# Performance work log

Hardware: AMD Instinct MI355X
Metric: run time of the kernel (lower is better)

Reference implementation:

```python
import jax, jax.numpy as jnp
import numpy as np

IMG = 1024
P0, P1 = 32, 16          # patch_size = [32, 16], P0 = 2*P1 required by stride-2 conv
C = 1                    # num_channels (must be 1 for unflatten(encoded, 1) to be valid)
N0 = (IMG // P0) ** 2    # 1024 patches at coarse scale
N1 = (IMG // P1) ** 2    # 4096 patches at fine scale
D0 = C * P0 * P0         # 1024 projection dim (coarse)
D1 = C * P1 * P1         # 256 projection dim (fine)
B = 8
BN_EPS = 1e-3            # keras BatchNormalization default
LRELU_ALPHA = 0.3        # keras LeakyReLU default


def setup_inputs() -> dict:
    key = jax.random.key(0)
    ks = jax.random.split(key, 9)
    return {
        "X": jax.random.normal(ks[0], (B, IMG, IMG, C), jnp.float32),
        "W_emb": jax.random.normal(ks[1], (N0, D0), jnp.float32) * 0.02,
        "conv_w": jax.random.normal(ks[2], (3, 3, N0, N1), jnp.float32) * 0.02,
        "conv_b": jnp.zeros((N1,), jnp.float32),
        "bn_gamma": jax.random.uniform(ks[3], (N1,), jnp.float32) + 0.5,
        "bn_beta": jax.random.normal(ks[4], (N1,), jnp.float32) * 0.1,
        "bn_mean": jax.random.normal(ks[5], (N1,), jnp.float32) * 0.1,
        "bn_var": jax.random.uniform(ks[6], (N1,), jnp.float32) + 0.5,
        "W_dense": jax.random.normal(ks[7], (D0, D0), jnp.float32) * 0.02,
        "b_dense": jnp.zeros((D0,), jnp.float32),
    }


def _patches(x, p):
    # [B,H,W,C] -> [B, (H/p)*(W/p), p, p, C]; row-major patch order, matching tf split/stack path.
    b, h, w, c = x.shape
    x = x.reshape(b, h // p, p, w // p, p, c).transpose(0, 1, 3, 2, 4, 5)
    return x.reshape(b, (h // p) * (w // p), p, p, c)


def _unpatch(x):
    # [B, n, p, p, C] -> [B, e*p, e*p, C] with e = sqrt(n); exact inverse of _patches.
    b, n, p, _, c = x.shape
    e = int(np.sqrt(n))
    x = x.reshape(b, e, e, p, p, c).transpose(0, 1, 3, 2, 4, 5)
    return x.reshape(b, e * p, e * p, c)


def reference(X, W_emb, conv_w, conv_b, bn_gamma, bn_beta, bn_mean, bn_var, W_dense, b_dense):
    b = X.shape[0]
    # fine-scale patches, flattened
    flat = _patches(X, P1).reshape(b, N1, D1)

    # positional embedding 1: positions = arange(N0) -> full embedding table
    pos1 = W_emb  # [N0, D0]

    # positional embedding 2: unflatten -> conv branch (inference: dropout = identity, BN uses moving stats)
    pe = pos1.reshape(1, N0, P0, P0, C).transpose(0, 4, 2, 3, 1).reshape(C, P0, P0, N0)  # [C,P0,P0,N0]
    y = jax.lax.conv_general_dilated(
        pe, conv_w, window_strides=(2, 2), padding='SAME',
        dimension_numbers=('NHWC', 'HWIO', 'NHWC')) + conv_b            # [C, P1, P1, N1]
    y = (y - bn_mean) * (bn_gamma / jnp.sqrt(bn_var + BN_EPS)) + bn_beta
    y = jnp.where(y > 0, y, LRELU_ALPHA * y)
    pos2 = y.reshape(1, C, P1, P1, N1).transpose(0, 4, 2, 3, 1).reshape(1, N1, D1)

    enc = flat + pos2                                                    # [B, N1, D1]
    # unflatten(.,1) -> unpatch -> repatch at coarse scale (pure reshape/transpose)
    img = _unpatch(enc.reshape(b, N1, P1, P1, 1))                        # [B, IMG, IMG, 1]
    enc = _patches(img, P0).reshape(b, N0, D0) + pos1                    # [B, N0, D0]
    return enc @ W_dense + b_dense
```

## Files before the change

### kernel.cpp

```cpp
#include <hip/hip_runtime.h>

typedef __attribute__((ext_vector_type(8))) short short8;
typedef __attribute__((ext_vector_type(4))) short short4v;
typedef __attribute__((ext_vector_type(4))) float float4v;

typedef const void __attribute__((address_space(1)))* gptr_t;
typedef void __attribute__((address_space(3)))* lptr_t;

__device__ __forceinline__ void gload_lds16(const void* g, void* l) {
    __builtin_amdgcn_global_load_lds((gptr_t)g, (lptr_t)l, 16, 0, 0);
}

__device__ __forceinline__ unsigned short f2bf(float f) {
    union { float f; unsigned int u; } v; v.f = f;
    unsigned int r = v.u + 0x7fffu + ((v.u >> 16) & 1u);
    return (unsigned short)(r >> 16);
}

__device__ __forceinline__ short8 frag_ld(const unsigned char* base, int row, int k2) {
    return *(const short8*)(base + row * 128 + (k2 ^ ((row & 7) << 4)));
}

__device__ __forceinline__ int swzB(int n) {
    return ((n ^ (n >> 3)) & 7) << 4;
}

__device__ __forceinline__ short8 frag_ldB(const unsigned char* base, int n, int k2) {
    return *(const short8*)(base + n * 128 + (k2 ^ swzB(n)));
}

__device__ __forceinline__ float4v mfma_bf16(short8 a, short8 b, float4v c) {
    return __builtin_amdgcn_mfma_f32_16x16x32_bf16(a, b, c, 0, 0, 0);
}

__global__ __launch_bounds__(256) void k_transpose_bf16(
        const float* __restrict__ in, unsigned short* __restrict__ out,
        float* __restrict__ zb) {
    __shared__ float tile[32][33];
    int tx = threadIdx.x, ty = threadIdx.y;
    if (blockIdx.x == 0 && blockIdx.y == 0 && ty == 0) zb[tx] = 0.0f;
    int x = blockIdx.x * 32 + tx;
    int ybase = blockIdx.y * 32;
#pragma unroll
    for (int j = 0; j < 4; j++)
        tile[ty + j * 8][tx] = in[(size_t)(ybase + ty + j * 8) * 1024 + x];
    __syncthreads();
    int ox = ybase + tx;
    int oybase = blockIdx.x * 32;
#pragma unroll
    for (int j = 0; j < 4; j++)
        out[(size_t)(oybase + ty + j * 8) * 1024 + ox] = f2bf(tile[tx][ty + j * 8]);
}

__global__ __launch_bounds__(256, 2) void k_conv_gemm(
        const float* __restrict__ convw,
        const unsigned short* __restrict__ peT,
        const unsigned short* __restrict__ zerobuf,
        float* __restrict__ y_part)
{
    __shared__ __align__(16) unsigned char ldsA[2][16384];
    __shared__ __align__(16) unsigned char ldsB[2][16384];

    const int t = threadIdx.x;
    const int L = blockIdx.x;
    const int ell = (L & 7) * 72 + (L >> 3);
    const int mt = ell & 1;
    const int nt = (ell >> 1) & 31;
    const int s  = ell >> 6;
    const int kh = s / 3, kw = s - kh * 3;
    const int ncol0 = nt * 128;

    const int l = t & 63, w = t >> 6;
    const int wm = w >> 1, wn = w & 1;
    const int l15 = l & 15;
    const int lk2 = (l >> 4) * 16;

    float4v acc[4][4] = {};

    const unsigned short* asrc[4];
    int aok[4];
#pragma unroll
    for (int i = 0; i < 4; i++) {
        int idx = i * 256 + t;
        int r = idx >> 3, c8 = idx & 7;
        int m = mt * 128 + r;
        int oh = m >> 4, ow = m & 15;
        int ih = 2 * oh + kh, iw = 2 * ow + kw;
        bool ok = (ih < 32) && (iw < 32);
        asrc[i] = ok ? (peT + (size_t)(ih * 32 + iw) * 1024 + ((c8 ^ (r & 7)) * 8))
                     : zerobuf;
        aok[i] = ok ? ~0 : 0;
    }

    const int a = t & 15, b = t >> 4;
    const float* bbase = convw + ((size_t)s * 1024 + 4 * a) * 4096 + ncol0 + 4 * b;

    float4v rb[2][2][4];

#pragma unroll
    for (int i = 0; i < 4; i++)
        gload_lds16(asrc[i], &ldsA[0][(i * 256 + t) * 16]);
#pragma unroll
    for (int c = 0; c < 2; c++)
#pragma unroll
        for (int j = 0; j < 4; j++)
            rb[0][c][j] = *(const float4v*)(bbase + (size_t)j * 4096 + c * 64);
    __builtin_amdgcn_sched_barrier(0);
#pragma unroll
    for (int i = 0; i < 4; i++)
        gload_lds16(asrc[i] + (64 & aok[i]), &ldsA[1][(i * 256 + t) * 16]);
#pragma unroll
    for (int c = 0; c < 2; c++)
#pragma unroll
        for (int j = 0; j < 4; j++)
            rb[1][c][j] = *(const float4v*)(bbase + (size_t)(64 + j) * 4096 + c * 64);
    asm volatile("s_waitcnt vmcnt(12)" ::: "memory");
    __builtin_amdgcn_sched_barrier(0);
#pragma unroll
    for (int c = 0; c < 2; c++)
#pragma unroll
        for (int i = 0; i < 4; i++) {
            int n = 4 * b + c * 64 + i;
            short4v v;
            v.x = (short)f2bf(rb[0][c][0][i]);
            v.y = (short)f2bf(rb[0][c][1][i]);
            v.z = (short)f2bf(rb[0][c][2][i]);
            v.w = (short)f2bf(rb[0][c][3][i]);
            *(short4v*)(&ldsB[0][n * 128 + ((a * 8) ^ swzB(n))]) = v;
        }
    asm volatile("s_waitcnt lgkmcnt(0)" ::: "memory");
    __builtin_amdgcn_s_barrier();

#pragma unroll
    for (int tt = 0; tt < 16; ++tt) {
        const int cur = tt & 1;

        short8 af[4][2], bfr[4][2];
#pragma unroll
        for (int mf = 0; mf < 4; mf++)
#pragma unroll
            for (int ks = 0; ks < 2; ks++)
                af[mf][ks] = frag_ld(ldsA[cur], wm * 64 + mf * 16 + l15, ks * 64 + lk2);
#pragma unroll
        for (int nf = 0; nf < 4; nf++)
#pragma unroll
            for (int ks = 0; ks < 2; ks++)
                bfr[nf][ks] = frag_ldB(ldsB[cur], wn * 64 + nf * 16 + l15, ks * 64 + lk2);
        asm volatile("s_waitcnt lgkmcnt(0)" ::: "memory");
        __builtin_amdgcn_sched_barrier(0);
        __builtin_amdgcn_s_barrier();
        __builtin_amdgcn_sched_barrier(0);

        if (tt < 14) {
            const int k0n = (tt + 2) * 64;
#pragma unroll
            for (int i = 0; i < 4; i++)
                gload_lds16(asrc[i] + (k0n & aok[i]), &ldsA[cur][(i * 256 + t) * 16]);
#pragma unroll
            for (int c = 0; c < 2; c++)
#pragma unroll
                for (int j = 0; j < 4; j++)
                    rb[cur][c][j] = *(const float4v*)(bbase + (size_t)(k0n + j) * 4096 + c * 64);
        }

        __builtin_amdgcn_s_setprio(1);
#pragma unroll
        for (int mf = 0; mf < 4; mf++)
#pragma unroll
            for (int nf = 0; nf < 4; nf++)
#pragma unroll
                for (int ks = 0; ks < 2; ks++)
                    acc[mf][nf] = mfma_bf16(af[mf][ks], bfr[nf][ks], acc[mf][nf]);
        __builtin_amdgcn_s_setprio(0);

        if (tt < 15) {
            if (tt < 14) asm volatile("s_waitcnt vmcnt(12)" ::: "memory");
            else         asm volatile("s_waitcnt vmcnt(0)" ::: "memory");
            __builtin_amdgcn_sched_barrier(0);
#pragma unroll
            for (int c = 0; c < 2; c++)
#pragma unroll
                for (int i = 0; i < 4; i++) {
                    int n = 4 * b + c * 64 + i;
                    short4v v;
                    v.x = (short)f2bf(rb[cur ^ 1][c][0][i]);
                    v.y = (short)f2bf(rb[cur ^ 1][c][1][i]);
                    v.z = (short)f2bf(rb[cur ^ 1][c][2][i]);
                    v.w = (short)f2bf(rb[cur ^ 1][c][3][i]);
                    *(short4v*)(&ldsB[cur ^ 1][n * 128 + ((a * 8) ^ swzB(n))]) = v;
                }
            asm volatile("s_waitcnt lgkmcnt(0)" ::: "memory");
            __builtin_amdgcn_sched_barrier(0);
            __builtin_amdgcn_s_barrier();
        }
    }

    float* yp = y_part + (size_t)s * 1048576;
#pragma unroll
    for (int mf = 0; mf < 4; mf++) {
        int row = mt * 128 + wm * 64 + mf * 16 + (l >> 4) * 4;
#pragma unroll
        for (int nf = 0; nf < 4; nf++) {
            int col = ncol0 + wn * 64 + nf * 16 + l15;
#pragma unroll
            for (int rr = 0; rr < 4; rr++)
                yp[(size_t)(row + rr) * 4096 + col] = acc[mf][nf][rr];
        }
    }
}

__global__ __launch_bounds__(256) void k_bn_pos2(
        const float* __restrict__ y_part, const float* __restrict__ cb,
        const float* __restrict__ gamma, const float* __restrict__ beta,
        const float* __restrict__ mean, const float* __restrict__ var,
        float* __restrict__ pos2img) {
    int idx = blockIdx.x * 256 + threadIdx.x;
    int m = idx >> 12, oc = idx & 4095;
    float v = cb[oc];
#pragma unroll
    for (int s = 0; s < 9; s++)
        v += y_part[(size_t)s * 1048576 + idx];
    v = (v - mean[oc]) * (gamma[oc] * rsqrtf(var[oc] + 1e-3f)) + beta[oc];
    v = v > 0.0f ? v : 0.3f * v;
    int y = ((oc >> 6) << 4) + (m >> 4);
    int x = ((oc & 63) << 4) + (m & 15);
    pos2img[y * 1024 + x] = v;
}

__global__ __launch_bounds__(256) void k_build_A(
        const float* __restrict__ X, const float* __restrict__ pos2img,
        const float* __restrict__ W_emb, unsigned short* __restrict__ Aenc) {
    int row = blockIdx.x;
    int n0 = row & 1023;
    int b  = row >> 10;
    int d0 = threadIdx.x * 4;
    int y = ((n0 >> 5) << 5) + (d0 >> 5);
    int x = ((n0 & 31) << 5) + (d0 & 31);
    size_t pix = (size_t)y * 1024 + x;
    float4v xv = *(const float4v*)(X + (size_t)b * 1048576 + pix);
    float4v pv = *(const float4v*)(pos2img + pix);
    float4v wv = *(const float4v*)(W_emb + (size_t)n0 * 1024 + d0);
    short4v o;
    o.x = (short)f2bf(xv.x + pv.x + wv.x);
    o.y = (short)f2bf(xv.y + pv.y + wv.y);
    o.z = (short)f2bf(xv.z + pv.z + wv.z);
    o.w = (short)f2bf(xv.w + pv.w + wv.w);
    *(short4v*)(Aenc + (size_t)row * 1024 + d0) = o;
}

__global__ __launch_bounds__(256) void k_final_gemm(
        const unsigned short* __restrict__ A,
        const unsigned short* __restrict__ Bt,
        const float* __restrict__ bias,
        float* __restrict__ C) {
    __shared__ __align__(16) unsigned char ldsA[16384];
    __shared__ __align__(16) unsigned char ldsB[16384];
    const int t = threadIdx.x;
    const int L = blockIdx.x;
    const int ell = (L & 7) * 64 + (L >> 3);
    const int col0 = (ell & 7) * 128;
    const int row0 = (ell >> 3) * 128;
    const int l = t & 63, w = t >> 6;
    const int wm = w >> 1, wn = w & 1;
    const int l15 = l & 15;
    const int lk2 = (l >> 4) * 16;

    float4v acc[4][4] = {};

    const unsigned short* asrc[4];
    const unsigned short* bsrc[4];
#pragma unroll
    for (int i = 0; i < 4; i++) {
        int idx = i * 256 + t;
        int r = idx >> 3, c8 = idx & 7;
        int cofs = (c8 ^ (r & 7)) * 8;
        asrc[i] = A  + (size_t)(row0 + r) * 1024 + cofs;
        bsrc[i] = Bt + (size_t)(col0 + r) * 1024 + cofs;
    }

    for (int k0 = 0; k0 < 1024; k0 += 64) {
#pragma unroll
        for (int i = 0; i < 4; i++) {
            int idx = i * 256 + t;
            gload_lds16(asrc[i] + k0, ldsA + idx * 16);
            gload_lds16(bsrc[i] + k0, ldsB + idx * 16);
        }
        __syncthreads();

        short8 af[4][2], bfr[4][2];
#pragma unroll
        for (int mf = 0; mf < 4; mf++)
#pragma unroll
            for (int ks = 0; ks < 2; ks++)
                af[mf][ks] = frag_ld(ldsA, wm * 64 + mf * 16 + l15, ks * 64 + lk2);
#pragma unroll
        for (int nf = 0; nf < 4; nf++)
#pragma unroll
            for (int ks = 0; ks < 2; ks++)
                bfr[nf][ks] = frag_ld(ldsB, wn * 64 + nf * 16 + l15, ks * 64 + lk2);
#pragma unroll
        for (int mf = 0; mf < 4; mf++)
#pragma unroll
            for (int nf = 0; nf < 4; nf++)
#pragma unroll
                for (int ks = 0; ks < 2; ks++)
                    acc[mf][nf] = mfma_bf16(af[mf][ks], bfr[nf][ks], acc[mf][nf]);
        __syncthreads();
    }

#pragma unroll
    for (int nf = 0; nf < 4; nf++) {
        int col = col0 + wn * 64 + nf * 16 + l15;
        float bv = bias[col];
#pragma unroll
        for (int mf = 0; mf < 4; mf++) {
            int row = row0 + wm * 64 + mf * 16 + (l >> 4) * 4;
#pragma unroll
            for (int r = 0; r < 4; r++)
                C[(size_t)(row + r) * 1024 + col] = acc[mf][nf][r] + bv;
        }
    }
}

extern "C" void kernel_launch(void* const* d_in, const int* in_sizes, int n_in,
                              void* d_out, int out_size, void* d_ws, size_t ws_size,
                              hipStream_t stream) {
    (void)in_sizes; (void)n_in; (void)out_size; (void)ws_size;
    const float* X       = (const float*)d_in[0];
    const float* W_emb   = (const float*)d_in[1];
    const float* conv_w  = (const float*)d_in[2];
    const float* conv_b  = (const float*)d_in[3];
    const float* gamma   = (const float*)d_in[4];
    const float* beta    = (const float*)d_in[5];
    const float* mean    = (const float*)d_in[6];
    const float* var     = (const float*)d_in[7];
    const float* W_dense = (const float*)d_in[8];
    const float* b_dense = (const float*)d_in[9];
    float* out = (float*)d_out;

    unsigned char* ws = (unsigned char*)d_ws;
    float*          y_part  = (float*)(ws);
    float*          zerobuf = (float*)(ws + (36u << 20));
    unsigned short* peT     = (unsigned short*)(ws + (38u << 20));
    unsigned short* WdT     = (unsigned short*)(ws + (40u << 20));
    float*          pos2img = (float*)(ws + (42u << 20));
    unsigned short* Aenc    = (unsigned short*)(ws + (48u << 20));

    dim3 tb(32, 8);
    k_transpose_bf16<<<dim3(32, 32), tb, 0, stream>>>(W_emb, peT, zerobuf);
    k_transpose_bf16<<<dim3(32, 32), tb, 0, stream>>>(W_dense, WdT, zerobuf);
    k_conv_gemm<<<576, 256, 0, stream>>>(conv_w, peT, (const unsigned short*)zerobuf, y_part);
    k_bn_pos2<<<4096, 256, 0, stream>>>(y_part, conv_b, gamma, beta, mean, var, pos2img);
    k_build_A<<<8192, 256, 0, stream>>>(X, pos2img, W_emb, Aenc);
    k_final_gemm<<<512, 256, 0, stream>>>(Aenc, WdT, b_dense, out);
}
```

Before: 131.8 us.

## Pre-convert conv weights to bf16 tiles in a separate kernel, read B fragments from global

```diff
diff --git a/kernel.cpp b/kernel.cpp
--- a/kernel.cpp
+++ b/kernel.cpp
@@ -19,14 +19,6 @@
 
 __device__ __forceinline__ short8 frag_ld(const unsigned char* base, int row, int k2) {
     return *(const short8*)(base + row * 128 + (k2 ^ ((row & 7) << 4)));
-}
-
-__device__ __forceinline__ int swzB(int n) {
-    return ((n ^ (n >> 3)) & 7) << 4;
-}
-
-__device__ __forceinline__ short8 frag_ldB(const unsigned char* base, int n, int k2) {
-    return *(const short8*)(base + n * 128 + (k2 ^ swzB(n)));
 }
 
 __device__ __forceinline__ float4v mfma_bf16(short8 a, short8 b, float4v c) {
@@ -52,21 +44,63 @@
         out[(size_t)(oybase + ty + j * 8) * 1024 + ox] = f2bf(tile[tx][ty + j * 8]);
 }
 
-__global__ __launch_bounds__(256, 2) void k_conv_gemm(
+__global__ __launch_bounds__(256) void k_prep_B(
         const float* __restrict__ convw,
+        unsigned short* __restrict__ Bprep, int sBase) {
+    __shared__ float ldsF[64][129];
+    const int t = threadIdx.x;
+    const int p = blockIdx.x;
+    const int step = p & 15;
+    const int nt   = (p >> 4) & 31;
+    const int sl   = p >> 9;
+    const int kglob = (sBase + sl) * 1024 + step * 64;
+
+    float4v rf[8];
+#pragma unroll
+    for (int j = 0; j < 8; j++) {
+        int r = j * 8 + (t >> 5);
+        int c4 = (t & 31) * 4;
+        rf[j] = *(const float4v*)(convw + (size_t)(kglob + r) * 4096 + nt * 128 + c4);
+    }
+#pragma unroll
+    for (int j = 0; j < 8; j++) {
+        int r = j * 8 + (t >> 5);
+        int c4 = (t & 31) * 4;
+#pragma unroll
+        for (int i = 0; i < 4; i++)
+            ldsF[r][c4 + i] = rf[j][i];
+    }
+    __syncthreads();
+
+    unsigned short* tile = Bprep + ((size_t)(sl * 32 + nt) * 16 + step) * 8192;
+#pragma unroll
+    for (int i = 0; i < 4; i++) {
+        int q = i * 256 + t;
+        int n = q >> 3, c8 = q & 7;
+        short8 o;
+#pragma unroll
+        for (int kk = 0; kk < 8; kk++)
+            o[kk] = (short)f2bf(ldsF[8 * c8 + kk][n]);
+        *(short8*)(tile + (size_t)q * 8) = o;
+    }
+}
+
+__global__ __launch_bounds__(256, 3) void k_conv_gemm(
         const unsigned short* __restrict__ peT,
         const unsigned short* __restrict__ zerobuf,
-        float* __restrict__ y_part)
+        const unsigned short* __restrict__ Bprep,
+        float* __restrict__ y_part, int sBase)
 {
     __shared__ __align__(16) unsigned char ldsA[2][16384];
-    __shared__ __align__(16) unsigned char ldsB[2][16384];
 
     const int t = threadIdx.x;
     const int L = blockIdx.x;
-    const int ell = (L & 7) * 72 + (L >> 3);
+    const int cpx = gridDim.x >> 3;
+    const int ell = (L & 7) * cpx + (L >> 3);
     const int mt = ell & 1;
     const int nt = (ell >> 1) & 31;
-    const int s  = ell >> 6;
+    const int sl = ell >> 6;
+    const int s  = sBase + sl;
     const int kh = s / 3, kw = s - kh * 3;
     const int ncol0 = nt * 128;
 
@@ -92,60 +126,40 @@
         aok[i] = ok ? ~0 : 0;
     }
 
-    const int a = t & 15, b = t >> 4;
-    const float* bbase = convw + ((size_t)s * 1024 + 4 * a) * 4096 + ncol0 + 4 * b;
-
-    float4v rb[2][2][4];
+    const unsigned char* Bt = (const unsigned char*)Bprep
+                            + (size_t)((sl * 32 + nt) * 16) * 16384;
 
 #pragma unroll
     for (int i = 0; i < 4; i++)
         gload_lds16(asrc[i], &ldsA[0][(i * 256 + t) * 16]);
-#pragma unroll
-    for (int c = 0; c < 2; c++)
-#pragma unroll
-        for (int j = 0; j < 4; j++)
-            rb[0][c][j] = *(const float4v*)(bbase + (size_t)j * 4096 + c * 64);
     __builtin_amdgcn_sched_barrier(0);
 #pragma unroll
     for (int i = 0; i < 4; i++)
         gload_lds16(asrc[i] + (64 & aok[i]), &ldsA[1][(i * 256 + t) * 16]);
-#pragma unroll
-    for (int c = 0; c < 2; c++)
-#pragma unroll
-        for (int j = 0; j < 4; j++)
-            rb[1][c][j] = *(const float4v*)(bbase + (size_t)(64 + j) * 4096 + c * 64);
-    asm volatile("s_waitcnt vmcnt(12)" ::: "memory");
+    asm volatile("s_waitcnt vmcnt(4)" ::: "memory");
     __builtin_amdgcn_sched_barrier(0);
-#pragma unroll
-    for (int c = 0; c < 2; c++)
-#pragma unroll
-        for (int i = 0; i < 4; i++) {
-            int n = 4 * b + c * 64 + i;
-            short4v v;
-            v.x = (short)f2bf(rb[0][c][0][i]);
-            v.y = (short)f2bf(rb[0][c][1][i]);
-            v.z = (short)f2bf(rb[0][c][2][i]);
-            v.w = (short)f2bf(rb[0][c][3][i]);
-            *(short4v*)(&ldsB[0][n * 128 + ((a * 8) ^ swzB(n))]) = v;
-        }
-    asm volatile("s_waitcnt lgkmcnt(0)" ::: "memory");
     __builtin_amdgcn_s_barrier();
 
 #pragma unroll
     for (int tt = 0; tt < 16; ++tt) {
         const int cur = tt & 1;
 
-        short8 af[4][2], bfr[4][2];
+        const unsigned char* tileT = Bt + tt * 16384;
+        short8 bfr[4][2];
+#pragma unroll
+        for (int nf = 0; nf < 4; nf++)
+#pragma unroll
+            for (int ks = 0; ks < 2; ks++)
+                bfr[nf][ks] = *(const short8*)(tileT
+                    + (wn * 64 + nf * 16 + l15) * 128 + (ks * 64 + lk2));
+        __builtin_amdgcn_sched_barrier(0);
+
+        short8 af[4][2];
 #pragma unroll
         for (int mf = 0; mf < 4; mf++)
 #pragma unroll
             for (int ks = 0; ks < 2; ks++)
                 af[mf][ks] = frag_ld(ldsA[cur], wm * 64 + mf * 16 + l15, ks * 64 + lk2);
-#pragma unroll
-        for (int nf = 0; nf < 4; nf++)
-#pragma unroll
-            for (int ks = 0; ks < 2; ks++)
-                bfr[nf][ks] = frag_ldB(ldsB[cur], wn * 64 + nf * 16 + l15, ks * 64 + lk2);
         asm volatile("s_waitcnt lgkmcnt(0)" ::: "memory");
         __builtin_amdgcn_sched_barrier(0);
         __builtin_amdgcn_s_barrier();
@@ -156,12 +170,11 @@
 #pragma unroll
             for (int i = 0; i < 4; i++)
                 gload_lds16(asrc[i] + (k0n & aok[i]), &ldsA[cur][(i * 256 + t) * 16]);
-#pragma unroll
-            for (int c = 0; c < 2; c++)
-#pragma unroll
-                for (int j = 0; j < 4; j++)
-                    rb[cur][c][j] = *(const float4v*)(bbase + (size_t)(k0n + j) * 4096 + c * 64);
         }
+        __builtin_amdgcn_sched_barrier(0);
+        if (tt < 14) asm volatile("s_waitcnt vmcnt(4)" ::: "memory");
+        else         asm volatile("s_waitcnt vmcnt(0)" ::: "memory");
+        __builtin_amdgcn_sched_barrier(0);
 
         __builtin_amdgcn_s_setprio(1);
 #pragma unroll
@@ -173,26 +186,7 @@
                     acc[mf][nf] = mfma_bf16(af[mf][ks], bfr[nf][ks], acc[mf][nf]);
         __builtin_amdgcn_s_setprio(0);
 
-        if (tt < 15) {
-            if (tt < 14) asm volatile("s_waitcnt vmcnt(12)" ::: "memory");
-            else         asm volatile("s_waitcnt vmcnt(0)" ::: "memory");
-            __builtin_amdgcn_sched_barrier(0);
-#pragma unroll
-            for (int c = 0; c < 2; c++)
-#pragma unroll
-                for (int i = 0; i < 4; i++) {
-                    int n = 4 * b + c * 64 + i;
-                    short4v v;
-                    v.x = (short)f2bf(rb[cur ^ 1][c][0][i]);
-                    v.y = (short)f2bf(rb[cur ^ 1][c][1][i]);
-                    v.z = (short)f2bf(rb[cur ^ 1][c][2][i]);
-                    v.w = (short)f2bf(rb[cur ^ 1][c][3][i]);
-                    *(short4v*)(&ldsB[cur ^ 1][n * 128 + ((a * 8) ^ swzB(n))]) = v;
-                }
-            asm volatile("s_waitcnt lgkmcnt(0)" ::: "memory");
-            __builtin_amdgcn_sched_barrier(0);
-            __builtin_amdgcn_s_barrier();
-        }
+        if (tt < 15) __builtin_amdgcn_s_barrier();
     }
 
     float* yp = y_part + (size_t)s * 1048576;
@@ -325,7 +319,7 @@
 extern "C" void kernel_launch(void* const* d_in, const int* in_sizes, int n_in,
                               void* d_out, int out_size, void* d_ws, size_t ws_size,
                               hipStream_t stream) {
-    (void)in_sizes; (void)n_in; (void)out_size; (void)ws_size;
+    (void)in_sizes; (void)n_in; (void)out_size;
     const float* X       = (const float*)d_in[0];
     const float* W_emb   = (const float*)d_in[1];
     const float* conv_w  = (const float*)d_in[2];
@@ -338,19 +332,29 @@
     const float* b_dense = (const float*)d_in[9];
     float* out = (float*)d_out;
 
+    const size_t MB = 1u << 20;
     unsigned char* ws = (unsigned char*)d_ws;
     float*          y_part  = (float*)(ws);
-    float*          zerobuf = (float*)(ws + (36u << 20));
-    unsigned short* peT     = (unsigned short*)(ws + (38u << 20));
-    unsigned short* WdT     = (unsigned short*)(ws + (40u << 20));
-    float*          pos2img = (float*)(ws + (42u << 20));
-    unsigned short* Aenc    = (unsigned short*)(ws + (48u << 20));
+    float*          zerobuf = (float*)(ws + 36 * MB);
+    unsigned short* peT     = (unsigned short*)(ws + 37 * MB);
+    unsigned short* Bprep   = (unsigned short*)(ws + 39 * MB);
+    float*          pos2img = (float*)(ws + 39 * MB);
+    unsigned short* Aenc    = (unsigned short*)(ws + 43 * MB);
+    unsigned short* WdT     = (unsigned short*)(ws + 59 * MB);
+
+    const int nCh    = (ws_size >= 112 * MB) ? 1 : 3;
+    const int sCount = (nCh == 1) ? 9 : 3;
 
     dim3 tb(32, 8);
     k_transpose_bf16<<<dim3(32, 32), tb, 0, stream>>>(W_emb, peT, zerobuf);
-    k_transpose_bf16<<<dim3(32, 32), tb, 0, stream>>>(W_dense, WdT, zerobuf);
-    k_conv_gemm<<<576, 256, 0, stream>>>(conv_w, peT, (const unsigned short*)zerobuf, y_part);
+    for (int c = 0; c < nCh; c++) {
+        int sBase = c * sCount;
+        k_prep_B<<<sCount * 512, 256, 0, stream>>>(conv_w, Bprep, sBase);
+        k_conv_gemm<<<sCount * 64, 256, 0, stream>>>(
+            peT, (const unsigned short*)zerobuf, Bprep, y_part, sBase);
+    }
     k_bn_pos2<<<4096, 256, 0, stream>>>(y_part, conv_b, gamma, beta, mean, var, pos2img);
     k_build_A<<<8192, 256, 0, stream>>>(X, pos2img, W_emb, Aenc);
+    k_transpose_bf16<<<dim3(32, 32), tb, 0, stream>>>(W_dense, WdT, zerobuf);
     k_final_gemm<<<512, 256, 0, stream>>>(Aenc, WdT, b_dense, out);
 }
```

After: 158.0 us. 1.2x slower.
